# Optimization experiments

Measured on AMD Instinct MI355X. Metric: run time of the kernel, lower is better.

The kernel has to match this reference:

```python
import math
import jax, jax.numpy as jnp
import numpy as np

HEADS = 4

def setup_inputs() -> dict:
    key = jax.random.key(0)
    ks = jax.random.split(key, 6)
    B, CK, CV, T, H, W = 2, 64, 512, 8, 32, 32
    return {
        "mk": jax.random.normal(ks[0], (B, CK, T, H, W), dtype=jnp.float32),
        "qk": jax.random.normal(ks[1], (B, CK, H, W), dtype=jnp.float32),
        "ms": jax.random.uniform(ks[2], (B, T, H, W), dtype=jnp.float32),
        "qe": jax.random.uniform(ks[3], (B, CK, H, W), dtype=jnp.float32),
        "mv": jax.random.normal(ks[4], (B, CV, T, H, W), dtype=jnp.float32),
        "qv": jax.random.normal(ks[5], (B, CV, H, W), dtype=jnp.float32),
    }

def reference(mk, qk, ms, qe, mv, qv):
    B, CK, T, H, W = mk.shape
    CV = mv.shape[1]
    THW, HW = T * H * W, H * W
    c = CK // HEADS

    # head split: [B, heads, c, THW] / [B, heads, c, HW]
    mk_h = mk.reshape(B, HEADS, c, THW)
    qk_h = qk.reshape(B, HEADS, c, HW)
    qe_h = qe.reshape(B, HEADS, c, HW)

    mk_t = jnp.swapaxes(mk_h, 2, 3)  # [B, heads, THW, c]
    # qe-weighted L2-style similarity with cubic terms
    a_sq = jnp.einsum('bhnc,bhcm->bhnm', mk_t ** 3, qe_h)          # [B,h,THW,HW]
    two_ab = 2.0 * jnp.einsum('bhnc,bhcm->bhnm', mk_t, qk_h * qe_h)
    b_sq = jnp.sum(qe_h * qk_h ** 3, axis=2, keepdims=True)        # [B,h,1,HW]
    similarity = -a_sq + two_ab - b_sq                              # [B,h,THW,HW]

    # shrinkage scaling: ms -> [B,1,THW,1], broadcast over heads
    similarity = similarity * ms.reshape(B, 1, THW, 1) / math.sqrt(CK)

    # softmax over the HEAD axis (dim=1), as in the original code
    affinity = jax.nn.softmax(similarity, axis=1)                   # [B,h,THW,HW]

    # readout: per-head batched matmul over memory positions
    mo = mv.reshape(B, HEADS, CV // HEADS, THW)
    mem = jnp.einsum('bhcn,bhnm->bhcm', mo, affinity).reshape(B, CV, H, W)
    return jnp.concatenate([mem, qv], axis=1)                       # [B, 2*CV, H, W]
```

## Files before the change

kernel.cpp:

```cpp
#include <hip/hip_runtime.h>

typedef float f4 __attribute__((ext_vector_type(4)));
typedef short s4 __attribute__((ext_vector_type(4)));
typedef short s8 __attribute__((ext_vector_type(8)));

#define HWD    1024
#define THW    8192
#define CVD    512
#define MT     32
#define NRANGE 1024
#define SUBS   32
#define AFP    36

#define MFMA16 __builtin_amdgcn_mfma_f32_16x16x32_bf16

__device__ __forceinline__ unsigned cvtpk(float a, float b) {
    unsigned r;
    asm volatile("v_cvt_pk_bf16_f32 %0, %1, %2" : "=v"(r) : "v"(a), "v"(b));
    return r;
}
__device__ __forceinline__ float ubits(unsigned u) {
    return __builtin_bit_cast(float, u);
}
__device__ __forceinline__ s8 frag2(const short* p) {
    return __builtin_shufflevector(*(const s4*)p, *(const s4*)(p + 4), 0,1,2,3,4,5,6,7);
}

__global__ __launch_bounds__(256)
void mr_prep(const float* __restrict__ mv, const float* __restrict__ qv,
             const float* __restrict__ mk,
             short* __restrict__ mvH, short* __restrict__ mvL,
             short* __restrict__ ftH, short* __restrict__ ftL,
             float* __restrict__ out)
{
    __shared__ float mkT[16][260];
    const int bid = blockIdx.x, t = threadIdx.x;
    if (bid < 8192) {
        int i = bid * 256 + t;
        f4 v = ((const f4*)mv)[i];
        unsigned h01 = cvtpk(v[0], v[1]);
        unsigned h23 = cvtpk(v[2], v[3]);
        float f0 = ubits(h01 << 16), f1 = ubits(h01 & 0xffff0000u);
        float f2 = ubits(h23 << 16), f3 = ubits(h23 & 0xffff0000u);
        unsigned l01 = cvtpk(v[0] - f0, v[1] - f1);
        unsigned l23 = cvtpk(v[2] - f2, v[3] - f3);
        ((uint2*)mvH)[i] = make_uint2(h01, h23);
        ((uint2*)mvL)[i] = make_uint2(l01, l23);
    } else if (bid < 10240) {
        int idx = (bid - 8192) * 256 + t;
        int b = idx >> 18, r = idx & 262143, ch = r >> 8;
        f4 v = f4{0.f, 0.f, 0.f, 0.f};
        if (ch >= CVD) v = ((const f4*)qv)[(b << 17) + ((ch - CVD) << 8) + (r & 255)];
        ((f4*)out)[idx] = v;
    } else {
        const int fbid = bid - 10240;
        const int chunk = fbid & 31, h = (fbid >> 5) & 3, b = fbid >> 7;
        const float* src = mk + (size_t)(b * 64 + h * 16) * THW + chunk * 256;
#pragma unroll
        for (int i = 0; i < 4; ++i) {
            int q = t + 256 * i;
            int c = q >> 6, j = q & 63;
            *(f4*)&mkT[c][j * 4] = *(const f4*)(src + (size_t)c * THW + j * 4);
        }
        __syncthreads();
        unsigned uH[16], uL[16];
#pragma unroll
        for (int c = 0; c < 16; ++c) {
            float x = mkT[c][t];
            float x3 = x * x * x;
            unsigned hh = cvtpk(x3, x);
            float r3 = x3 - ubits(hh << 16);
            float r1 = x  - ubits(hh & 0xffff0000u);
            uH[c] = hh;
            uL[c] = cvtpk(r3, r1);
        }
        size_t row = ((size_t)(b * 4 + h) * THW + chunk * 256 + t) * 32;
        uint4* dH = (uint4*)(ftH + row);
        uint4* dL = (uint4*)(ftL + row);
#pragma unroll
        for (int k = 0; k < 4; ++k) {
            dH[k] = make_uint4(uH[4*k], uH[4*k+1], uH[4*k+2], uH[4*k+3]);
            dL[k] = make_uint4(uL[4*k], uL[4*k+1], uL[4*k+2], uL[4*k+3]);
        }
    }
}

__global__ __launch_bounds__(256, 4)
void mr_main(const float* __restrict__ qk, const float* __restrict__ qe,
             const float* __restrict__ ms,
             const short* __restrict__ mvH, const short* __restrict__ mvL,
             const short* __restrict__ ftH, const short* __restrict__ ftL,
             float* __restrict__ out)
{
    union SM {
        struct { short wH[4][MT][AFP]; } su;
        struct { short aff[2][2][MT][AFP]; float msv[NRANGE]; } mn;
    };
    __shared__ __align__(16) SM sm;
    __shared__ __align__(16) short wLs[4][MT][AFP];
    __shared__ float bS[4][MT];

    const int bid  = blockIdx.x;
    const int wid  = (bid & 7) * 128 + (bid >> 3);
    const int nc   = wid >> 7;
    const int rest = wid & 127;
    const int mt0  = rest & 31;
    const int hp   = (rest >> 5) & 1;
    const int b    = rest >> 6;
    const int m0   = mt0 * MT;
    const int n0   = nc * NRANGE;

    const int t  = threadIdx.x;
    const int wv = t >> 6, l = t & 63, lr = l & 15, lg = l >> 4;
    const int nt = wv & 1, mq = wv >> 1;
    const int hl = wv & 1, cvh = wv >> 1;

    if (t < 128) {
        const int h = t >> 5, m = t & 31;
        const float* qkp = qk + (size_t)(b * 64 + h * 16) * HWD + m0 + m;
        const float* qep = qe + (size_t)(b * 64 + h * 16) * HWD + m0 + m;
        float bias = 0.f;
#pragma unroll
        for (int c = 0; c < 16; ++c) {
            float kv = qkp[(size_t)c * HWD];
            float ev = qep[(size_t)c * HWD];
            float w0 = -ev, w1 = 2.f * kv * ev;
            unsigned hh = cvtpk(w0, w1);
            float r0 = w0 - ubits(hh << 16);
            float r1 = w1 - ubits(hh & 0xffff0000u);
            *(unsigned*)&sm.su.wH[h][m][2 * c] = hh;
            *(unsigned*)&wLs[h][m][2 * c]      = cvtpk(r0, r1);
            bias -= ev * kv * kv * kv;
        }
        bS[h][m] = bias;
    }
    __syncthreads();

    s8 wHr[4];
    float biasr[4];
#pragma unroll
    for (int h = 0; h < 4; ++h) {
        wHr[h]   = frag2(&sm.su.wH[h][mq * 16 + lr][lg * 8]);
        biasr[h] = bS[h][mq * 16 + lr];
    }
    ((f4*)sm.mn.msv)[t] = ((const f4*)(ms + (size_t)b * THW + n0))[t];
    __syncthreads();

    f4 acc[4][2];
#pragma unroll
    for (int ct = 0; ct < 4; ++ct) {
        acc[ct][0] = f4{0.f, 0.f, 0.f, 0.f};
        acc[ct][1] = f4{0.f, 0.f, 0.f, 0.f};
    }

    const size_t fstep  = (size_t)THW * 32;
    const short* fbaseH = ftH + ((size_t)(b * 4) * THW + n0 + nt * 16 + lr) * 32 + lg * 8;
    const short* fbaseL = ftL + ((size_t)(b * 4) * THW + n0 + nt * 16 + lr) * 32 + lg * 8;
    const size_t abase0 = ((size_t)(b * CVD + hp * 256 + hl * 128 + cvh * 64 + lr)) * THW
                          + n0 + lg * 8;

    for (int s = 0; s < SUBS; ++s) {
        const int ns = s * 32;

        f4 sacc[4];
#pragma unroll
        for (int h = 0; h < 4; ++h) {
            s8 fH = *(const s8*)(fbaseH + (size_t)h * fstep + (size_t)ns * 32);
            s8 fL = *(const s8*)(fbaseL + (size_t)h * fstep + (size_t)ns * 32);
            s8 wL = frag2(&wLs[h][mq * 16 + lr][lg * 8]);
            f4 sa = f4{biasr[h], biasr[h], biasr[h], biasr[h]};
            sa = MFMA16(fH, wHr[h], sa, 0, 0, 0);
            sa = MFMA16(fL, wHr[h], sa, 0, 0, 0);
            sa = MFMA16(fH, wL,     sa, 0, 0, 0);
            sacc[h] = sa;
        }

        s8 aHr[4], aLr[4];
#pragma unroll
        for (int ct = 0; ct < 4; ++ct) {
            size_t ao = abase0 + (size_t)ct * 16 * THW + ns;
            aHr[ct] = *(const s8*)(mvH + ao);
            aLr[ct] = *(const s8*)(mvL + ao);
        }

        f4 msv4 = *(const f4*)&sm.mn.msv[ns + nt * 16 + lg * 4];
        float a0[4], a1[4];
#pragma unroll
        for (int r = 0; r < 4; ++r) {
            const float sc = msv4[r] * 0.125f;
            float x0 = sacc[0][r] * sc, x1 = sacc[1][r] * sc;
            float x2 = sacc[2][r] * sc, x3 = sacc[3][r] * sc;
            float mx = fmaxf(fmaxf(x0, x1), fmaxf(x2, x3));
            float e0 = __expf(x0 - mx), e1 = __expf(x1 - mx);
            float e2 = __expf(x2 - mx), e3 = __expf(x3 - mx);
            float rin = 1.f / (e0 + e1 + e2 + e3);
            a0[r] = (hp ? e2 : e0) * rin;
            a1[r] = (hp ? e3 : e1) * rin;
        }
        unsigned h001 = cvtpk(a0[0], a0[1]), h023 = cvtpk(a0[2], a0[3]);
        unsigned h101 = cvtpk(a1[0], a1[1]), h123 = cvtpk(a1[2], a1[3]);
        unsigned l001 = cvtpk(a0[0] - ubits(h001 << 16), a0[1] - ubits(h001 & 0xffff0000u));
        unsigned l023 = cvtpk(a0[2] - ubits(h023 << 16), a0[3] - ubits(h023 & 0xffff0000u));
        unsigned l101 = cvtpk(a1[0] - ubits(h101 << 16), a1[1] - ubits(h101 & 0xffff0000u));
        unsigned l123 = cvtpk(a1[2] - ubits(h123 << 16), a1[3] - ubits(h123 & 0xffff0000u));
        {
            const int mrow = mq * 16 + lr, nn = nt * 16 + lg * 4;
            *(uint2*)&sm.mn.aff[0][0][mrow][nn] = make_uint2(h001, h023);
            *(uint2*)&sm.mn.aff[1][0][mrow][nn] = make_uint2(l001, l023);
            *(uint2*)&sm.mn.aff[0][1][mrow][nn] = make_uint2(h101, h123);
            *(uint2*)&sm.mn.aff[1][1][mrow][nn] = make_uint2(l101, l123);
        }
        __syncthreads();

        s8 bH[2], bL[2];
#pragma unroll
        for (int mt = 0; mt < 2; ++mt) {
            bH[mt] = frag2(&sm.mn.aff[0][hl][mt * 16 + lr][lg * 8]);
            bL[mt] = frag2(&sm.mn.aff[1][hl][mt * 16 + lr][lg * 8]);
        }
#pragma unroll
        for (int ct = 0; ct < 4; ++ct)
#pragma unroll
            for (int mt = 0; mt < 2; ++mt) {
                acc[ct][mt] = MFMA16(aHr[ct], bH[mt], acc[ct][mt], 0, 0, 0);
                acc[ct][mt] = MFMA16(aLr[ct], bH[mt], acc[ct][mt], 0, 0, 0);
                acc[ct][mt] = MFMA16(aHr[ct], bL[mt], acc[ct][mt], 0, 0, 0);
            }
        __syncthreads();
    }

    float* ob = out + (size_t)b * (2 * CVD * HWD);
#pragma unroll
    for (int ct = 0; ct < 4; ++ct)
#pragma unroll
        for (int mt = 0; mt < 2; ++mt)
#pragma unroll
            for (int r = 0; r < 4; ++r) {
                const int cv = hp * 256 + hl * 128 + cvh * 64 + ct * 16 + lg * 4 + r;
                const int m  = m0 + mt * 16 + lr;
#if defined(__HIP_PLATFORM_AMD__)
                unsafeAtomicAdd(ob + (size_t)cv * HWD + m, acc[ct][mt][r]);
#else
                atomicAdd(ob + (size_t)cv * HWD + m, acc[ct][mt][r]);
#endif
            }
}

extern "C" void kernel_launch(void* const* d_in, const int* in_sizes, int n_in,
                              void* d_out, int out_size, void* d_ws, size_t ws_size,
                              hipStream_t stream) {
    (void)in_sizes; (void)n_in; (void)out_size; (void)ws_size;
    const float* mk = (const float*)d_in[0];
    const float* qk = (const float*)d_in[1];
    const float* ms = (const float*)d_in[2];
    const float* qe = (const float*)d_in[3];
    const float* mv = (const float*)d_in[4];
    const float* qv = (const float*)d_in[5];
    float* out = (float*)d_out;

    short* mvH = (short*)d_ws;
    short* mvL = (short*)((char*)d_ws + 16777216);
    short* ftH = (short*)((char*)d_ws + 33554432);
    short* ftL = (short*)((char*)d_ws + 37748736);

    mr_prep<<<10496, 256, 0, stream>>>(mv, qv, mk, mvH, mvL, ftH, ftL, out);
    mr_main<<<1024, 256, 0, stream>>>(qk, qe, ms, mvH, mvL, ftH, ftL, out);
}
```

Before: 302.9 us.

## Restructure readout to keep affinity in registers and drop value low-part split

Memory values are now stored only as a single bf16 high part, with no low-residual array, which halves value traffic and removes one MFMA per readout product. The main kernel moves to 512-thread blocks that each cover a 2048-wide memory range. Each wave feeds its softmax output straight into 16x16x16 MFMAs from registers, so there is no LDS round-trip and no per-step barriers. The ms scale factor is folded into shared memory up front. This trades precision on the value operand (bf16 only) and a different work split for less bandwidth and fewer syncs.

```diff
diff --git a/kernel.cpp b/kernel.cpp
--- a/kernel.cpp
+++ b/kernel.cpp
@@ -3,33 +3,47 @@
 typedef float f4 __attribute__((ext_vector_type(4)));
 typedef short s4 __attribute__((ext_vector_type(4)));
 typedef short s8 __attribute__((ext_vector_type(8)));
-
-#define HWD    1024
-#define THW    8192
-#define CVD    512
-#define MT     32
-#define NRANGE 1024
-#define SUBS   32
-#define AFP    36
-
-#define MFMA16 __builtin_amdgcn_mfma_f32_16x16x32_bf16
-
-__device__ __forceinline__ unsigned cvtpk(float a, float b) {
-    unsigned r;
+typedef unsigned u32;
+
+#define HWD 1024
+#define THW 8192
+#define CVD 512
+#define AFP 36
+
+#define MFMA32 __builtin_amdgcn_mfma_f32_16x16x32_bf16
+
+__device__ __forceinline__ f4 mfma1616(s4 a, s4 b, f4 c) {
+#if __has_builtin(__builtin_amdgcn_mfma_f32_16x16x16_bf16)
+    return __builtin_amdgcn_mfma_f32_16x16x16_bf16(a, b, c, 0, 0, 0);
+#elif __has_builtin(__builtin_amdgcn_mfma_f32_16x16x16bf16_1k)
+    return __builtin_amdgcn_mfma_f32_16x16x16bf16_1k(a, b, c, 0, 0, 0);
+#else
+    f4 d;
+    asm volatile("v_mfma_f32_16x16x16_bf16 %0, %1, %2, %3"
+                 : "=v"(d) : "v"(a), "v"(b), "v"(c));
+    return d;
+#endif
+}
+
+__device__ __forceinline__ u32 cvtpk(float a, float b) {
+    u32 r;
     asm volatile("v_cvt_pk_bf16_f32 %0, %1, %2" : "=v"(r) : "v"(a), "v"(b));
     return r;
 }
-__device__ __forceinline__ float ubits(unsigned u) {
+__device__ __forceinline__ float ubits(u32 u) {
     return __builtin_bit_cast(float, u);
 }
 __device__ __forceinline__ s8 frag2(const short* p) {
     return __builtin_shufflevector(*(const s4*)p, *(const s4*)(p + 4), 0,1,2,3,4,5,6,7);
+}
+__device__ __forceinline__ s4 pks4(u32 a, u32 b) {
+    return __builtin_bit_cast(s4, make_uint2(a, b));
 }
 
 __global__ __launch_bounds__(256)
 void mr_prep(const float* __restrict__ mv, const float* __restrict__ qv,
              const float* __restrict__ mk,
-             short* __restrict__ mvH, short* __restrict__ mvL,
+             short* __restrict__ mvH,
              short* __restrict__ ftH, short* __restrict__ ftL,
              float* __restrict__ out)
 {
@@ -38,14 +52,7 @@
     if (bid < 8192) {
         int i = bid * 256 + t;
         f4 v = ((const f4*)mv)[i];
-        unsigned h01 = cvtpk(v[0], v[1]);
-        unsigned h23 = cvtpk(v[2], v[3]);
-        float f0 = ubits(h01 << 16), f1 = ubits(h01 & 0xffff0000u);
-        float f2 = ubits(h23 << 16), f3 = ubits(h23 & 0xffff0000u);
-        unsigned l01 = cvtpk(v[0] - f0, v[1] - f1);
-        unsigned l23 = cvtpk(v[2] - f2, v[3] - f3);
-        ((uint2*)mvH)[i] = make_uint2(h01, h23);
-        ((uint2*)mvL)[i] = make_uint2(l01, l23);
+        ((uint2*)mvH)[i] = make_uint2(cvtpk(v[0], v[1]), cvtpk(v[2], v[3]));
     } else if (bid < 10240) {
         int idx = (bid - 8192) * 256 + t;
         int b = idx >> 18, r = idx & 262143, ch = r >> 8;
@@ -63,12 +70,12 @@
             *(f4*)&mkT[c][j * 4] = *(const f4*)(src + (size_t)c * THW + j * 4);
         }
         __syncthreads();
-        unsigned uH[16], uL[16];
+        u32 uH[16], uL[16];
 #pragma unroll
         for (int c = 0; c < 16; ++c) {
             float x = mkT[c][t];
             float x3 = x * x * x;
-            unsigned hh = cvtpk(x3, x);
+            u32 hh = cvtpk(x3, x);
             float r3 = x3 - ubits(hh << 16);
             float r1 = x  - ubits(hh & 0xffff0000u);
             uH[c] = hh;
@@ -85,35 +92,32 @@
     }
 }
 
-__global__ __launch_bounds__(256, 4)
+__global__ __launch_bounds__(512, 4)
 void mr_main(const float* __restrict__ qk, const float* __restrict__ qe,
              const float* __restrict__ ms,
-             const short* __restrict__ mvH, const short* __restrict__ mvL,
+             const short* __restrict__ mvH,
              const short* __restrict__ ftH, const short* __restrict__ ftL,
              float* __restrict__ out)
 {
-    union SM {
-        struct { short wH[4][MT][AFP]; } su;
-        struct { short aff[2][2][MT][AFP]; float msv[NRANGE]; } mn;
-    };
-    __shared__ __align__(16) SM sm;
-    __shared__ __align__(16) short wLs[4][MT][AFP];
-    __shared__ float bS[4][MT];
+    __shared__ __align__(16) short wSH[4][32][AFP];
+    __shared__ __align__(16) short wSL[4][32][AFP];
+    __shared__ float msS[2048];
+    __shared__ float bS[4][32];
 
     const int bid  = blockIdx.x;
-    const int wid  = (bid & 7) * 128 + (bid >> 3);
-    const int nc   = wid >> 7;
+    const int wid  = (bid & 7) * 64 + (bid >> 3);
+    const int ncg  = wid >> 7;
     const int rest = wid & 127;
     const int mt0  = rest & 31;
     const int hp   = (rest >> 5) & 1;
     const int b    = rest >> 6;
-    const int m0   = mt0 * MT;
-    const int n0   = nc * NRANGE;
+    const int m0   = mt0 * 32;
+    const int n0   = ncg * 2048;
 
     const int t  = threadIdx.x;
     const int wv = t >> 6, l = t & 63, lr = l & 15, lg = l >> 4;
-    const int nt = wv & 1, mq = wv >> 1;
-    const int hl = wv & 1, cvh = wv >> 1;
+    const int ws = wv & 3;
+    const int wm = wv >> 2;
 
     if (t < 128) {
         const int h = t >> 5, m = t & 31;
@@ -125,14 +129,18 @@
             float kv = qkp[(size_t)c * HWD];
             float ev = qep[(size_t)c * HWD];
             float w0 = -ev, w1 = 2.f * kv * ev;
-            unsigned hh = cvtpk(w0, w1);
+            u32 hh = cvtpk(w0, w1);
             float r0 = w0 - ubits(hh << 16);
             float r1 = w1 - ubits(hh & 0xffff0000u);
-            *(unsigned*)&sm.su.wH[h][m][2 * c] = hh;
-            *(unsigned*)&wLs[h][m][2 * c]      = cvtpk(r0, r1);
+            *(u32*)&wSH[h][m][2 * c] = hh;
+            *(u32*)&wSL[h][m][2 * c] = cvtpk(r0, r1);
             bias -= ev * kv * kv * kv;
         }
         bS[h][m] = bias;
+    }
+    {
+        f4 v = ((const f4*)(ms + (size_t)b * THW + n0))[t];
+        ((f4*)msS)[t] = v * 0.125f;
     }
     __syncthreads();
 
@@ -140,56 +148,41 @@
     float biasr[4];
 #pragma unroll
     for (int h = 0; h < 4; ++h) {
-        wHr[h]   = frag2(&sm.su.wH[h][mq * 16 + lr][lg * 8]);
-        biasr[h] = bS[h][mq * 16 + lr];
-    }
-    ((f4*)sm.mn.msv)[t] = ((const f4*)(ms + (size_t)b * THW + n0))[t];
-    __syncthreads();
-
-    f4 acc[4][2];
-#pragma unroll
-    for (int ct = 0; ct < 4; ++ct) {
-        acc[ct][0] = f4{0.f, 0.f, 0.f, 0.f};
-        acc[ct][1] = f4{0.f, 0.f, 0.f, 0.f};
-    }
-
-    const size_t fstep  = (size_t)THW * 32;
-    const short* fbaseH = ftH + ((size_t)(b * 4) * THW + n0 + nt * 16 + lr) * 32 + lg * 8;
-    const short* fbaseL = ftL + ((size_t)(b * 4) * THW + n0 + nt * 16 + lr) * 32 + lg * 8;
-    const size_t abase0 = ((size_t)(b * CVD + hp * 256 + hl * 128 + cvh * 64 + lr)) * THW
-                          + n0 + lg * 8;
-
-    for (int s = 0; s < SUBS; ++s) {
-        const int ns = s * 32;
+        wHr[h]   = frag2(&wSH[h][wm * 16 + lr][lg * 8]);
+        biasr[h] = bS[h][wm * 16 + lr];
+    }
+
+    f4 acc[16];
+#pragma unroll
+    for (int ct = 0; ct < 16; ++ct) acc[ct] = f4{0.f, 0.f, 0.f, 0.f};
+
+    const int nb0 = n0 + ws * 512;
+    const short* fbH = ftH + ((size_t)(b * 4) * THW + nb0 + lr) * 32 + lg * 8;
+    const short* fbL = ftL + ((size_t)(b * 4) * THW + nb0 + lr) * 32 + lg * 8;
+    const short* mvb = mvH + (size_t)(b * CVD + hp * 256 + lr) * THW + nb0 + lg * 4;
+
+    for (int s = 0; s < 32; ++s) {
+        const int nn = s * 16;
 
         f4 sacc[4];
 #pragma unroll
         for (int h = 0; h < 4; ++h) {
-            s8 fH = *(const s8*)(fbaseH + (size_t)h * fstep + (size_t)ns * 32);
-            s8 fL = *(const s8*)(fbaseL + (size_t)h * fstep + (size_t)ns * 32);
-            s8 wL = frag2(&wLs[h][mq * 16 + lr][lg * 8]);
+            s8 fH = *(const s8*)(fbH + (size_t)h * (THW * 32) + nn * 32);
+            s8 fL = *(const s8*)(fbL + (size_t)h * (THW * 32) + nn * 32);
+            s8 wL = frag2(&wSL[h][wm * 16 + lr][lg * 8]);
             f4 sa = f4{biasr[h], biasr[h], biasr[h], biasr[h]};
-            sa = MFMA16(fH, wHr[h], sa, 0, 0, 0);
-            sa = MFMA16(fL, wHr[h], sa, 0, 0, 0);
-            sa = MFMA16(fH, wL,     sa, 0, 0, 0);
+            sa = MFMA32(fH, wHr[h], sa, 0, 0, 0);
+            sa = MFMA32(fL, wHr[h], sa, 0, 0, 0);
+            sa = MFMA32(fH, wL,     sa, 0, 0, 0);
             sacc[h] = sa;
         }
 
-        s8 aHr[4], aLr[4];
-#pragma unroll
-        for (int ct = 0; ct < 4; ++ct) {
-            size_t ao = abase0 + (size_t)ct * 16 * THW + ns;
-            aHr[ct] = *(const s8*)(mvH + ao);
-            aLr[ct] = *(const s8*)(mvL + ao);
-        }
-
-        f4 msv4 = *(const f4*)&sm.mn.msv[ns + nt * 16 + lg * 4];
+        f4 msv = *(const f4*)&msS[ws * 512 + nn + lg * 4];
         float a0[4], a1[4];
 #pragma unroll
         for (int r = 0; r < 4; ++r) {
-            const float sc = msv4[r] * 0.125f;
-            float x0 = sacc[0][r] * sc, x1 = sacc[1][r] * sc;
-            float x2 = sacc[2][r] * sc, x3 = sacc[3][r] * sc;
+            float x0 = sacc[0][r] * msv[r], x1 = sacc[1][r] * msv[r];
+            float x2 = sacc[2][r] * msv[r], x3 = sacc[3][r] * msv[r];
             float mx = fmaxf(fmaxf(x0, x1), fmaxf(x2, x3));
             float e0 = __expf(x0 - mx), e1 = __expf(x1 - mx);
             float e2 = __expf(x2 - mx), e3 = __expf(x3 - mx);
@@ -197,53 +190,36 @@
             a0[r] = (hp ? e2 : e0) * rin;
             a1[r] = (hp ? e3 : e1) * rin;
         }
-        unsigned h001 = cvtpk(a0[0], a0[1]), h023 = cvtpk(a0[2], a0[3]);
-        unsigned h101 = cvtpk(a1[0], a1[1]), h123 = cvtpk(a1[2], a1[3]);
-        unsigned l001 = cvtpk(a0[0] - ubits(h001 << 16), a0[1] - ubits(h001 & 0xffff0000u));
-        unsigned l023 = cvtpk(a0[2] - ubits(h023 << 16), a0[3] - ubits(h023 & 0xffff0000u));
-        unsigned l101 = cvtpk(a1[0] - ubits(h101 << 16), a1[1] - ubits(h101 & 0xffff0000u));
-        unsigned l123 = cvtpk(a1[2] - ubits(h123 << 16), a1[3] - ubits(h123 & 0xffff0000u));
-        {
-            const int mrow = mq * 16 + lr, nn = nt * 16 + lg * 4;
-            *(uint2*)&sm.mn.aff[0][0][mrow][nn] = make_uint2(h001, h023);
-            *(uint2*)&sm.mn.aff[1][0][mrow][nn] = make_uint2(l001, l023);
-            *(uint2*)&sm.mn.aff[0][1][mrow][nn] = make_uint2(h101, h123);
-            *(uint2*)&sm.mn.aff[1][1][mrow][nn] = make_uint2(l101, l123);
-        }
-        __syncthreads();
-
-        s8 bH[2], bL[2];
-#pragma unroll
-        for (int mt = 0; mt < 2; ++mt) {
-            bH[mt] = frag2(&sm.mn.aff[0][hl][mt * 16 + lr][lg * 8]);
-            bL[mt] = frag2(&sm.mn.aff[1][hl][mt * 16 + lr][lg * 8]);
-        }
-#pragma unroll
-        for (int ct = 0; ct < 4; ++ct)
-#pragma unroll
-            for (int mt = 0; mt < 2; ++mt) {
-                acc[ct][mt] = MFMA16(aHr[ct], bH[mt], acc[ct][mt], 0, 0, 0);
-                acc[ct][mt] = MFMA16(aLr[ct], bH[mt], acc[ct][mt], 0, 0, 0);
-                acc[ct][mt] = MFMA16(aHr[ct], bL[mt], acc[ct][mt], 0, 0, 0);
-            }
-        __syncthreads();
-    }
-
-    float* ob = out + (size_t)b * (2 * CVD * HWD);
-#pragma unroll
-    for (int ct = 0; ct < 4; ++ct)
-#pragma unroll
-        for (int mt = 0; mt < 2; ++mt)
-#pragma unroll
-            for (int r = 0; r < 4; ++r) {
-                const int cv = hp * 256 + hl * 128 + cvh * 64 + ct * 16 + lg * 4 + r;
-                const int m  = m0 + mt * 16 + lr;
+        u32 p001 = cvtpk(a0[0], a0[1]), p023 = cvtpk(a0[2], a0[3]);
+        u32 p101 = cvtpk(a1[0], a1[1]), p123 = cvtpk(a1[2], a1[3]);
+        s4 bH0 = pks4(p001, p023);
+        s4 bH1 = pks4(p101, p123);
+        s4 bL0 = pks4(cvtpk(a0[0] - ubits(p001 << 16), a0[1] - ubits(p001 & 0xffff0000u)),
+                      cvtpk(a0[2] - ubits(p023 << 16), a0[3] - ubits(p023 & 0xffff0000u)));
+        s4 bL1 = pks4(cvtpk(a1[0] - ubits(p101 << 16), a1[1] - ubits(p101 & 0xffff0000u)),
+                      cvtpk(a1[2] - ubits(p123 << 16), a1[3] - ubits(p123 & 0xffff0000u)));
+
+#pragma unroll
+        for (int ct = 0; ct < 16; ++ct) {
+            s4 aH = *(const s4*)(mvb + (size_t)ct * 16 * THW + nn);
+            s4 bh = (ct < 8) ? bH0 : bH1;
+            s4 bl = (ct < 8) ? bL0 : bL1;
+            acc[ct] = mfma1616(aH, bh, acc[ct]);
+            acc[ct] = mfma1616(aH, bl, acc[ct]);
+        }
+    }
+
+    float* ob = out + (size_t)b * (2 * CVD * HWD)
+                + (size_t)(hp * 256) * HWD + m0 + wm * 16 + lr;
+#pragma unroll
+    for (int ct = 0; ct < 16; ++ct)
+#pragma unroll
+        for (int r = 0; r < 4; ++r)
 #if defined(__HIP_PLATFORM_AMD__)
-                unsafeAtomicAdd(ob + (size_t)cv * HWD + m, acc[ct][mt][r]);
+            unsafeAtomicAdd(ob + (size_t)(ct * 16 + lg * 4 + r) * HWD, acc[ct][r]);
 #else
-                atomicAdd(ob + (size_t)cv * HWD + m, acc[ct][mt][r]);
+            atomicAdd(ob + (size_t)(ct * 16 + lg * 4 + r) * HWD, acc[ct][r]);
 #endif
-            }
 }
 
 extern "C" void kernel_launch(void* const* d_in, const int* in_sizes, int n_in,
@@ -259,10 +235,9 @@
     float* out = (float*)d_out;
 
     short* mvH = (short*)d_ws;
-    short* mvL = (short*)((char*)d_ws + 16777216);
-    short* ftH = (short*)((char*)d_ws + 33554432);
-    short* ftL = (short*)((char*)d_ws + 37748736);
-
-    mr_prep<<<10496, 256, 0, stream>>>(mv, qv, mk, mvH, mvL, ftH, ftL, out);
-    mr_main<<<1024, 256, 0, stream>>>(qk, qe, ms, mvH, mvL, ftH, ftL, out);
-}
+    short* ftH = (short*)((char*)d_ws + 16777216);
+    short* ftL = (short*)((char*)d_ws + 20971520);
+
+    mr_prep<<<10496, 256, 0, stream>>>(mv, qv, mk, mvH, ftH, ftL, out);
+    mr_main<<<512, 512, 0, stream>>>(qk, qe, ms, mvH, ftH, ftL, out);
+}
```

After: 439.7 us. 1.45x slower.
